# Performance work log

Measured on AMD Instinct MI355X. Metric: run time of the kernel, lower is better.

The kernel has to match this reference:

```python
import jax, jax.numpy as jnp
import numpy as np

N_NODES = 100000
N_EDGES = 1280000
IN_DIM = 256
OUT_DIM = 64


def setup_inputs() -> dict:
    key = jax.random.key(0)
    k1, k2, k3, k4, k5, k6 = jax.random.split(key, 6)
    x = jax.random.normal(k1, (N_NODES, IN_DIM), dtype=jnp.float32)
    support_rows = jax.random.randint(k2, (N_EDGES,), 0, N_NODES, dtype=jnp.int64)
    support_cols = jax.random.randint(k3, (N_EDGES,), 0, N_NODES, dtype=jnp.int64)
    support_vals = jax.random.uniform(k4, (N_EDGES,), dtype=jnp.float32)
    weight = jax.random.normal(k5, (IN_DIM, OUT_DIM), dtype=jnp.float32) * 0.05
    bias = jax.random.normal(k6, (OUT_DIM,), dtype=jnp.float32) * 0.05
    return {
        "x": x,
        "support_rows": support_rows,
        "support_cols": support_cols,
        "support_vals": support_vals,
        "weight": weight,
        "bias": bias,
    }


def reference(x, support_rows, support_cols, support_vals, weight, bias):
    # dropout=0, training=False -> dropout is identity
    # pre_sup = X @ W : [N, out_dim]
    pre_sup = jnp.matmul(x, weight)
    # sparse support (COO) @ pre_sup : gather source rows, scale, scatter-add to dest rows
    gathered = pre_sup[support_cols] * support_vals[:, None]  # [E, out_dim]
    out = jax.ops.segment_sum(gathered, support_rows, num_segments=N_NODES)
    out = out + bias
    return jax.nn.relu(out)
```

## Files before the change

### kernel.cpp

```cpp
#include <hip/hip_runtime.h>
#include <hip/hip_bf16.h>
#include <stdint.h>

#define N_NODES 100000
#define N_EDGES 1280000
#define IN_DIM  256
#define OUT_DIM 64
#define NB1     98
#define GEMM_BLOCKS ((N_NODES + 63) / 64)
#define PART_SZ 12500

typedef __attribute__((ext_vector_type(8))) short bf16x8;
typedef __attribute__((ext_vector_type(4))) float f32x4;
typedef __attribute__((ext_vector_type(4))) unsigned short u16x4;

__device__ __forceinline__ unsigned short f32_to_bf16(float f) {
    union { float f; unsigned int u; } c; c.f = f;
    unsigned int u = c.u;
    u += 0x7fffu + ((u >> 16) & 1u);
    return (unsigned short)(u >> 16);
}
__device__ __forceinline__ float bf16_to_f32(unsigned short h) {
    union { unsigned int u; float f; } c; c.u = ((unsigned int)h) << 16; return c.f;
}

__global__ __launch_bounds__(256) void gemm_hist_kernel(const float* __restrict__ x,
                                                        const float* __restrict__ w,
                                                        unsigned short* __restrict__ pre,
                                                        const int* __restrict__ rows,
                                                        int* __restrict__ deg) {
    __shared__ __align__(16) unsigned short wt[8 * 4 * 64 * 8];
    __shared__ __align__(16) unsigned short xs[4][8][4][136];

    const int tid = threadIdx.x;

    for (int i = tid; i < IN_DIM * OUT_DIM; i += 256) {
        const int k = i >> 6, n = i & 63;
        const int kt = k >> 5, q = (k >> 3) & 3, j = k & 7;
        const int t = n >> 4, l = n & 15;
        wt[((kt * 4 + t) * 64 + q * 16 + l) * 8 + j] = f32_to_bf16(w[i]);
    }

    const int R0 = blockIdx.x * 64;
    #pragma unroll
    for (int it = 0; it < 16; ++it) {
        const int flatv = it * 256 + tid;
        const int r  = flatv >> 6;
        const int k4 = (flatv & 63) * 4;
        int gr = R0 + r; gr = gr < N_NODES ? gr : N_NODES - 1;
        f32x4 xv = *(const f32x4*)(x + (size_t)gr * IN_DIM + k4);
        const int kt = k4 >> 5, q = (k4 >> 3) & 3, j = k4 & 7;
        u16x4 pk;
        pk[0] = f32_to_bf16(xv.x); pk[1] = f32_to_bf16(xv.y);
        pk[2] = f32_to_bf16(xv.z); pk[3] = f32_to_bf16(xv.w);
        *(u16x4*)&xs[r >> 4][kt][q][(r & 15) * 8 + j] = pk;
    }
    __syncthreads();

    const int wave = tid >> 6;
    const int lane = tid & 63;
    const int ln16 = lane & 15;
    const int quad = lane >> 4;

    f32x4 acc[4] = {};

    #pragma unroll
    for (int kt = 0; kt < 8; ++kt) {
        bf16x8 a = *(const bf16x8*)&xs[wave][kt][quad][ln16 * 8];
        #pragma unroll
        for (int t = 0; t < 4; ++t) {
            bf16x8 b = *(const bf16x8*)(&wt[((kt * 4 + t) * 64 + lane) * 8]);
            acc[t] = __builtin_amdgcn_mfma_f32_16x16x32_bf16(a, b, acc[t], 0, 0, 0);
        }
    }

    const int rbase = R0 + wave * 16 + quad * 4;
    #pragma unroll
    for (int t = 0; t < 4; ++t) {
        #pragma unroll
        for (int r = 0; r < 4; ++r) {
            const int rr = rbase + r;
            if (rr < N_NODES)
                pre[(size_t)rr * OUT_DIM + t * 16 + ln16] = f32_to_bf16(acc[t][r]);
        }
    }

    for (int e = blockIdx.x * 256 + tid; e < N_EDGES; e += GEMM_BLOCKS * 256) {
        atomicAdd(&deg[rows[e]], 1);
    }
}

__global__ __launch_bounds__(256) void scan1_kernel(const int* __restrict__ deg,
                                                    int* __restrict__ off,
                                                    int* __restrict__ bsum) {
    __shared__ int s[256];
    const int t = threadIdx.x;
    const int base = blockIdx.x * 1024 + t * 4;
    int d[4];
    #pragma unroll
    for (int q = 0; q < 4; ++q) {
        const int i = base + q;
        d[q] = i < N_NODES ? deg[i] : 0;
    }
    const int tsum = d[0] + d[1] + d[2] + d[3];
    s[t] = tsum;
    __syncthreads();
    #pragma unroll
    for (int o = 1; o < 256; o <<= 1) {
        const int add = t >= o ? s[t - o] : 0;
        __syncthreads();
        s[t] += add;
        __syncthreads();
    }
    int run = t > 0 ? s[t - 1] : 0;
    #pragma unroll
    for (int q = 0; q < 4; ++q) {
        const int i = base + q;
        if (i < N_NODES) off[i] = run;
        run += d[q];
    }
    if (t == 255) bsum[blockIdx.x] = run;
}

__global__ __launch_bounds__(128) void scan2_kernel(const int* __restrict__ bsum,
                                                    int* __restrict__ boff,
                                                    int* __restrict__ off) {
    __shared__ int s[128];
    const int t = threadIdx.x;
    const int v = t < NB1 ? bsum[t] : 0;
    s[t] = v;
    __syncthreads();
    #pragma unroll
    for (int o = 1; o < 128; o <<= 1) {
        const int add = t >= o ? s[t - o] : 0;
        __syncthreads();
        s[t] += add;
        __syncthreads();
    }
    if (t < NB1) boff[t] = t > 0 ? s[t - 1] : 0;
    if (t == 127) off[N_NODES] = s[127];
}

__global__ __launch_bounds__(256) void scan3_kernel(int* __restrict__ off,
                                                    const int* __restrict__ boff,
                                                    int* __restrict__ cursor) {
    const int i = blockIdx.x * 256 + threadIdx.x;
    if (i < N_NODES) {
        const int v = off[i] + boff[i >> 10];
        off[i] = v;
        cursor[i] = v;
    }
}

__global__ __launch_bounds__(256) void reorder_kernel(const int* __restrict__ rows,
                                                      const int* __restrict__ cols,
                                                      const float* __restrict__ vals,
                                                      int* __restrict__ cursor,
                                                      unsigned long long* __restrict__ epack) {
    const int part = blockIdx.x & 7;
    const int lo = part * PART_SZ;
    const int hi = lo + PART_SZ;
    const int base = (blockIdx.x >> 3) * 2048 + threadIdx.x;
    #pragma unroll
    for (int k = 0; k < 8; ++k) {
        const int e = base + k * 256;
        const int r = rows[e];
        if (r >= lo && r < hi) {
            const int c = cols[e];
            const float v = vals[e];
            const int slot = atomicAdd(&cursor[r], 1);
            epack[slot] = ((unsigned long long)__float_as_uint(v) << 32) | (unsigned int)c;
        }
    }
}

__global__ __launch_bounds__(256) void gather_kernel(const int* __restrict__ off,
                                                     const unsigned long long* __restrict__ epack,
                                                     const unsigned short* __restrict__ pre,
                                                     const float* __restrict__ bias,
                                                     float* __restrict__ out) {
    const int v = blockIdx.x * 4 + (threadIdx.x >> 6);
    const int j = threadIdx.x & 63;
    if (v >= N_NODES) return;
    const int s = off[v];
    const int e = off[v + 1];
    float acc = 0.0f;
    int i = s;
    for (; i + 4 <= e; i += 4) {
        unsigned long long ee[4];
        float p[4];
        #pragma unroll
        for (int q = 0; q < 4; ++q) ee[q] = epack[i + q];
        #pragma unroll
        for (int q = 0; q < 4; ++q)
            p[q] = bf16_to_f32(pre[(size_t)(unsigned int)(ee[q] & 0xffffffffu) * OUT_DIM + j]);
        #pragma unroll
        for (int q = 0; q < 4; ++q)
            acc = fmaf(p[q], __uint_as_float((unsigned int)(ee[q] >> 32)), acc);
    }
    for (; i < e; ++i) {
        const unsigned long long e0 = epack[i];
        acc = fmaf(bf16_to_f32(pre[(size_t)(unsigned int)(e0 & 0xffffffffu) * OUT_DIM + j]),
                   __uint_as_float((unsigned int)(e0 >> 32)), acc);
    }
    const float r = acc + bias[j];
    out[(size_t)v * OUT_DIM + j] = r > 0.0f ? r : 0.0f;
}

extern "C" void kernel_launch(void* const* d_in, const int* in_sizes, int n_in,
                              void* d_out, int out_size, void* d_ws, size_t ws_size,
                              hipStream_t stream) {
    const float* x    = (const float*)d_in[0];
    const int* rows   = (const int*)d_in[1];
    const int* cols   = (const int*)d_in[2];
    const float* vals = (const float*)d_in[3];
    const float* w    = (const float*)d_in[4];
    const float* bias = (const float*)d_in[5];
    float* out        = (float*)d_out;

    unsigned short* pre = (unsigned short*)d_ws;
    int* deg    = (int*)(pre + (size_t)N_NODES * OUT_DIM);
    int* off    = deg + N_NODES;
    int* cursor = off + N_NODES + 2;
    int* bsum   = cursor + N_NODES;
    int* boff   = bsum + 128;
    unsigned long long* epack = (unsigned long long*)(boff + 128);

    hipMemsetAsync(deg, 0, N_NODES * sizeof(int), stream);

    gemm_hist_kernel<<<GEMM_BLOCKS, 256, 0, stream>>>(x, w, pre, rows, deg);

    scan1_kernel<<<NB1, 256, 0, stream>>>(deg, off, bsum);
    scan2_kernel<<<1, 128, 0, stream>>>(bsum, boff, off);
    scan3_kernel<<<(N_NODES + 255) / 256, 256, 0, stream>>>(off, boff, cursor);

    reorder_kernel<<<5000, 256, 0, stream>>>(rows, cols, vals, cursor, epack);

    gather_kernel<<<(N_NODES + 3) / 4, 256, 0, stream>>>(off, epack, pre, bias, out);
}
```

Baseline: 345.0 us.

## Prepack bf16 weights once and load X directly into MFMA registers

The hipMemsetAsync is replaced by a small kernel that zeroes the degree array and, in block 0, converts and packs the weights to bf16 once into workspace (aliased onto the cursor buffer). The GEMM kernel then copies the prepacked weights into LDS with vector loads instead of converting per block. It also reads X straight from global memory into registers for the MFMA A operand, dropping the LDS staging buffer and one barrier. This cuts LDS use and per-block conversion work and adds an occupancy hint of 5, at the cost of less coalesced X loads and an extra kernel launch.

```diff
diff --git a/kernel.cpp b/kernel.cpp
--- a/kernel.cpp
+++ b/kernel.cpp
@@ -24,52 +24,64 @@
     union { unsigned int u; float f; } c; c.u = ((unsigned int)h) << 16; return c.f;
 }
 
-__global__ __launch_bounds__(256) void gemm_hist_kernel(const float* __restrict__ x,
-                                                        const float* __restrict__ w,
-                                                        unsigned short* __restrict__ pre,
-                                                        const int* __restrict__ rows,
-                                                        int* __restrict__ deg) {
-    __shared__ __align__(16) unsigned short wt[8 * 4 * 64 * 8];
-    __shared__ __align__(16) unsigned short xs[4][8][4][136];
-
+__global__ __launch_bounds__(256) void wpack_zero_kernel(const float* __restrict__ w,
+                                                         unsigned short* __restrict__ wbf,
+                                                         int* __restrict__ deg) {
     const int tid = threadIdx.x;
-
-    for (int i = tid; i < IN_DIM * OUT_DIM; i += 256) {
-        const int k = i >> 6, n = i & 63;
-        const int kt = k >> 5, q = (k >> 3) & 3, j = k & 7;
-        const int t = n >> 4, l = n & 15;
-        wt[((kt * 4 + t) * 64 + q * 16 + l) * 8 + j] = f32_to_bf16(w[i]);
-    }
-
-    const int R0 = blockIdx.x * 64;
-    #pragma unroll
-    for (int it = 0; it < 16; ++it) {
-        const int flatv = it * 256 + tid;
-        const int r  = flatv >> 6;
-        const int k4 = (flatv & 63) * 4;
-        int gr = R0 + r; gr = gr < N_NODES ? gr : N_NODES - 1;
-        f32x4 xv = *(const f32x4*)(x + (size_t)gr * IN_DIM + k4);
-        const int kt = k4 >> 5, q = (k4 >> 3) & 3, j = k4 & 7;
-        u16x4 pk;
-        pk[0] = f32_to_bf16(xv.x); pk[1] = f32_to_bf16(xv.y);
-        pk[2] = f32_to_bf16(xv.z); pk[3] = f32_to_bf16(xv.w);
-        *(u16x4*)&xs[r >> 4][kt][q][(r & 15) * 8 + j] = pk;
-    }
-    __syncthreads();
+    const int base = blockIdx.x * 1024 + tid * 4;
+    #pragma unroll
+    for (int q = 0; q < 4; ++q) {
+        const int i = base + q;
+        if (i < N_NODES) deg[i] = 0;
+    }
+    if (blockIdx.x == 0) {
+        for (int i = tid; i < IN_DIM * OUT_DIM; i += 256) {
+            const int k = i >> 6, n = i & 63;
+            const int kt = k >> 5, q = (k >> 3) & 3, j = k & 7;
+            const int t = n >> 4, l = n & 15;
+            wbf[((kt * 4 + t) * 64 + q * 16 + l) * 8 + j] = f32_to_bf16(w[i]);
+        }
+    }
+}
+
+__global__ __launch_bounds__(256, 5) void gemm_hist_kernel(const float* __restrict__ x,
+                                                           const unsigned short* __restrict__ wbf,
+                                                           unsigned short* __restrict__ pre,
+                                                           const int* __restrict__ rows,
+                                                           int* __restrict__ deg) {
+    __shared__ __align__(16) unsigned short wt[IN_DIM * OUT_DIM];
+
+    const int tid = threadIdx.x;
+
+    #pragma unroll
+    for (int i = 0; i < 8; ++i)
+        *(bf16x8*)&wt[i * 2048 + tid * 8] = *(const bf16x8*)(wbf + i * 2048 + tid * 8);
 
     const int wave = tid >> 6;
     const int lane = tid & 63;
     const int ln16 = lane & 15;
     const int quad = lane >> 4;
 
+    const int R0 = blockIdx.x * 64;
+    const int arow = R0 + wave * 16 + ln16;
+    const float* xrow = x + (size_t)(arow < N_NODES ? arow : N_NODES - 1) * IN_DIM + quad * 8;
+
+    __syncthreads();
+
     f32x4 acc[4] = {};
 
     #pragma unroll
     for (int kt = 0; kt < 8; ++kt) {
-        bf16x8 a = *(const bf16x8*)&xs[wave][kt][quad][ln16 * 8];
+        f32x4 xa = *(const f32x4*)(xrow + kt * 32);
+        f32x4 xb = *(const f32x4*)(xrow + kt * 32 + 4);
+        bf16x8 a;
+        a[0] = (short)f32_to_bf16(xa.x); a[1] = (short)f32_to_bf16(xa.y);
+        a[2] = (short)f32_to_bf16(xa.z); a[3] = (short)f32_to_bf16(xa.w);
+        a[4] = (short)f32_to_bf16(xb.x); a[5] = (short)f32_to_bf16(xb.y);
+        a[6] = (short)f32_to_bf16(xb.z); a[7] = (short)f32_to_bf16(xb.w);
         #pragma unroll
         for (int t = 0; t < 4; ++t) {
-            bf16x8 b = *(const bf16x8*)(&wt[((kt * 4 + t) * 64 + lane) * 8]);
+            bf16x8 b = *(const bf16x8*)&wt[((kt * 4 + t) * 64 + lane) * 8];
             acc[t] = __builtin_amdgcn_mfma_f32_16x16x32_bf16(a, b, acc[t], 0, 0, 0);
         }
     }
@@ -221,14 +233,16 @@
     unsigned short* pre = (unsigned short*)d_ws;
     int* deg    = (int*)(pre + (size_t)N_NODES * OUT_DIM);
     int* off    = deg + N_NODES;
-    int* cursor = off + N_NODES + 2;
+    int* cursor = off + N_NODES + 4;
     int* bsum   = cursor + N_NODES;
     int* boff   = bsum + 128;
     unsigned long long* epack = (unsigned long long*)(boff + 128);
 
-    hipMemsetAsync(deg, 0, N_NODES * sizeof(int), stream);
-
-    gemm_hist_kernel<<<GEMM_BLOCKS, 256, 0, stream>>>(x, w, pre, rows, deg);
+    unsigned short* wbf = (unsigned short*)cursor;
+
+    wpack_zero_kernel<<<NB1, 256, 0, stream>>>(w, wbf, deg);
+
+    gemm_hist_kernel<<<GEMM_BLOCKS, 256, 0, stream>>>(x, wbf, pre, rows, deg);
 
     scan1_kernel<<<NB1, 256, 0, stream>>>(deg, off, bsum);
     scan2_kernel<<<1, 128, 0, stream>>>(bsum, boff, off);
```

Measured after the change: 348.7 us. Within noise of the previous version (+1.1%).
